# Performance work log

Measured on AMD Instinct MI355X. Metric: run time of the kernel, lower is better.

The kernel has to match this reference:

```python
import jax, jax.numpy as jnp
import numpy as np

ATT_SIZE = 32
HEAD_NUM = 2


def setup_inputs() -> dict:
    key = jax.random.key(0)
    k_in, k_q, k_k, k_v, k_r = jax.random.split(key, 5)
    B, F, D = 16384, 32, 64
    H = ATT_SIZE * HEAD_NUM  # 64
    inputs = jax.random.normal(k_in, (B, F, D), dtype=jnp.float32)
    W_Query = jax.random.truncated_normal(k_q, -2.0, 2.0, (D, H), dtype=jnp.float32) * 0.05
    W_Key = jax.random.truncated_normal(k_k, -2.0, 2.0, (D, H), dtype=jnp.float32) * 0.05
    W_Value = jax.random.truncated_normal(k_v, -2.0, 2.0, (D, H), dtype=jnp.float32) * 0.05
    W_Res = jax.random.truncated_normal(k_r, -2.0, 2.0, (D, H), dtype=jnp.float32) * 0.05
    return {"inputs": inputs, "W_Query": W_Query, "W_Key": W_Key, "W_Value": W_Value, "W_Res": W_Res}


def reference(inputs, W_Query, W_Key, W_Value, W_Res):
    B, F, D = inputs.shape
    h, a = HEAD_NUM, ATT_SIZE
    # project and reshape to [B, h, F, a]
    q = jnp.einsum('bfd,de->bfe', inputs, W_Query).reshape(B, F, h, a).transpose(0, 2, 1, 3)
    k = jnp.einsum('bfd,de->bfe', inputs, W_Key).reshape(B, F, h, a).transpose(0, 2, 1, 3)
    v = jnp.einsum('bfd,de->bfe', inputs, W_Value).reshape(B, F, h, a).transpose(0, 2, 1, 3)
    # NOTE: original code has NO 1/sqrt(d) scaling
    scores = jnp.einsum('bhqa,bhka->bhqk', q, k)
    attn = jax.nn.softmax(scores, axis=-1)
    out = jnp.einsum('bhqk,bhka->bhqa', attn, v)  # [B, h, F, a]
    out = out.transpose(0, 2, 1, 3).reshape(B, F, h * a)
    out = out + jnp.einsum('bfd,de->bfe', inputs, W_Res)
    return jax.nn.relu(out)
```

## Files before the change

kernel.cpp:

```cpp
#include <hip/hip_runtime.h>


constexpr int kF = 32, kD = 64, kH = 64;

using short8   = __attribute__((ext_vector_type(8))) short;
using float4v  = __attribute__((ext_vector_type(4))) float;
using ushort4v = __attribute__((ext_vector_type(4))) unsigned short;

__device__ __forceinline__ unsigned short f2bf(float x) {
    return __builtin_bit_cast(unsigned short, (__bf16)x);
}
__device__ __forceinline__ float bf2f(unsigned short b) {
    return __uint_as_float((unsigned)b << 16);
}
__device__ __forceinline__ int sw64(int row, int blk) {
    return blk ^ ((row ^ (row >> 1)) & 7);
}
__device__ __forceinline__ int sw32(int row, int blk) {
    return blk ^ ((row ^ (row >> 2)) & 3);
}

__global__ void wprep_kernel(const float* __restrict__ Wq, const float* __restrict__ Wk,
                             const float* __restrict__ Wv, const float* __restrict__ Wr,
                             unsigned short* __restrict__ wt) {
    const int m = blockIdx.x;
    const float* __restrict__ W = (m == 0) ? Wq : (m == 1) ? Wk : (m == 2) ? Wv : Wr;
    for (int i = threadIdx.x; i < kD * kH; i += blockDim.x) {
        const int e = i >> 6, d = i & 63;
        wt[m * kD * kH + e * kD + d] = f2bf(W[d * kH + e]);
    }
}

__global__ __launch_bounds__(256, 8)
void interact_mfma(const float* __restrict__ X, const unsigned short* __restrict__ Wt,
                   float* __restrict__ out)
{
    __shared__ __align__(16) unsigned short s_xp[2048];
    __shared__ __align__(16) unsigned short s_q [2048];
    __shared__ __align__(16) unsigned short s_k [2048];
    __shared__ __align__(16) unsigned short s_vt[2048];
    __shared__ __align__(16) unsigned short s_rt[2048];

    const int t    = threadIdx.x;
    const int w    = t >> 6;
    const int lane = t & 63;
    const int quad = lane >> 4;
    const int l    = lane & 15;
    const int b    = blockIdx.x;
    const int h    = w >> 1;
    const int wmt  = w & 1;

    short8 bfrag[4][2];
    {
        const unsigned short* __restrict__ wtm = Wt + w * (kD * kH);
        #pragma unroll
        for (int nt = 0; nt < 4; ++nt)
            #pragma unroll
            for (int ks = 0; ks < 2; ++ks)
                bfrag[nt][ks] =
                    *reinterpret_cast<const short8*>(wtm + (16 * nt + l) * kD + 32 * ks + quad * 8);
    }

    const float* __restrict__ Xb = X + (size_t)b * (kF * kD);
    #pragma unroll
    for (int i = 0; i < 2; ++i) {
        const int idx = i * 256 + t;
        const int f = idx >> 4, c = idx & 15;
        const float4 v = reinterpret_cast<const float4*>(Xb)[idx];
        ushort4v pk = { f2bf(v.x), f2bf(v.y), f2bf(v.z), f2bf(v.w) };
        *reinterpret_cast<ushort4v*>(
            &s_xp[f * 64 + sw64(f, c >> 1) * 8 + (c & 1) * 4]) = pk;
    }
    __syncthreads();

    {
        short8 afrag[2][2];
        #pragma unroll
        for (int mt = 0; mt < 2; ++mt)
            #pragma unroll
            for (int ks = 0; ks < 2; ++ks) {
                const int row = 16 * mt + l;
                afrag[mt][ks] = *reinterpret_cast<const short8*>(
                    &s_xp[row * 64 + sw64(row, 4 * ks + quad) * 8]);
            }

        float4v acc[2][4];
        #pragma unroll
        for (int mt = 0; mt < 2; ++mt)
            #pragma unroll
            for (int nt = 0; nt < 4; ++nt)
                acc[mt][nt] = (float4v){0.f, 0.f, 0.f, 0.f};

        #pragma unroll
        for (int mt = 0; mt < 2; ++mt)
            #pragma unroll
            for (int nt = 0; nt < 4; ++nt) {
                acc[mt][nt] = __builtin_amdgcn_mfma_f32_16x16x32_bf16(
                    afrag[mt][0], bfrag[nt][0], acc[mt][nt], 0, 0, 0);
                acc[mt][nt] = __builtin_amdgcn_mfma_f32_16x16x32_bf16(
                    afrag[mt][1], bfrag[nt][1], acc[mt][nt], 0, 0, 0);
            }

        if (w < 2) {
            unsigned short* __restrict__ dst = (w == 0) ? s_q : s_k;
            #pragma unroll
            for (int mt = 0; mt < 2; ++mt)
                #pragma unroll
                for (int nt = 0; nt < 4; ++nt)
                    #pragma unroll
                    for (int r = 0; r < 4; ++r) {
                        const int row = 16 * mt + quad * 4 + r;
                        dst[row * 64 + sw64(row, 2 * nt + (l >> 3)) * 8 + (l & 7)] =
                            f2bf(acc[mt][nt][r]);
                    }
        } else {
            unsigned short* __restrict__ dstT = (w == 2) ? s_vt : s_rt;
            #pragma unroll
            for (int mt = 0; mt < 2; ++mt)
                #pragma unroll
                for (int nt = 0; nt < 4; ++nt) {
                    const int e = 16 * nt + l;
                    ushort4v pk = { f2bf(acc[mt][nt][0]), f2bf(acc[mt][nt][1]),
                                    f2bf(acc[mt][nt][2]), f2bf(acc[mt][nt][3]) };
                    *reinterpret_cast<ushort4v*>(
                        &dstT[e * 32 + sw32(e, 2 * mt + (quad >> 1)) * 8 + (quad & 1) * 4]) = pk;
                }
        }
    }
    __syncthreads();

    {
        const int qrow = 16 * wmt + l;
        const short8 qa = *reinterpret_cast<const short8*>(
            &s_q[qrow * 64 + sw64(qrow, 4 * h + quad) * 8]);
        const short8 kb0 = *reinterpret_cast<const short8*>(
            &s_k[l * 64 + sw64(l, 4 * h + quad) * 8]);
        const short8 kb1 = *reinterpret_cast<const short8*>(
            &s_k[(16 + l) * 64 + sw64(16 + l, 4 * h + quad) * 8]);

        float4v s0 = (float4v){0.f, 0.f, 0.f, 0.f};
        float4v s1 = (float4v){0.f, 0.f, 0.f, 0.f};
        s0 = __builtin_amdgcn_mfma_f32_16x16x32_bf16(qa, kb0, s0, 0, 0, 0);
        s1 = __builtin_amdgcn_mfma_f32_16x16x32_bf16(qa, kb1, s1, 0, 0, 0);

        #pragma unroll
        for (int r = 0; r < 4; ++r) {
            const int rowG = h * kF + 16 * wmt + quad * 4 + r;
            s_xp[rowG * 32 + sw32(rowG, l >> 3) * 8 + (l & 7)]       = f2bf(__expf(s0[r]));
            s_xp[rowG * 32 + sw32(rowG, 2 + (l >> 3)) * 8 + (l & 7)] = f2bf(__expf(s1[r]));
        }
    }

    {
        const int prow = h * kF + 16 * wmt + l;
        const short8 pa = *reinterpret_cast<const short8*>(
            &s_xp[prow * 32 + sw32(prow, quad) * 8]);
        const short8 vb0 = *reinterpret_cast<const short8*>(
            &s_vt[(32 * h + l) * 32 + sw32(32 * h + l, quad) * 8]);
        const short8 vb1 = *reinterpret_cast<const short8*>(
            &s_vt[(32 * h + 16 + l) * 32 + sw32(32 * h + 16 + l, quad) * 8]);
        const short8 ones = (short8)(short)0x3F80;

        float4v o0 = (float4v){0.f, 0.f, 0.f, 0.f};
        float4v o1 = (float4v){0.f, 0.f, 0.f, 0.f};
        float4v os = (float4v){0.f, 0.f, 0.f, 0.f};
        o0 = __builtin_amdgcn_mfma_f32_16x16x32_bf16(pa, vb0, o0, 0, 0, 0);
        o1 = __builtin_amdgcn_mfma_f32_16x16x32_bf16(pa, vb1, o1, 0, 0, 0);
        os = __builtin_amdgcn_mfma_f32_16x16x32_bf16(pa, ones, os, 0, 0, 0);

        const ushort4v rA = *reinterpret_cast<const ushort4v*>(
            &s_rt[(32 * h + l) * 32 + sw32(32 * h + l, 2 * wmt + (quad >> 1)) * 8 + (quad & 1) * 4]);
        const ushort4v rB = *reinterpret_cast<const ushort4v*>(
            &s_rt[(32 * h + 16 + l) * 32 + sw32(32 * h + 16 + l, 2 * wmt + (quad >> 1)) * 8 + (quad & 1) * 4]);

        float* __restrict__ Ob = out + (size_t)b * (kF * kH);
        #pragma unroll
        for (int r = 0; r < 4; ++r) {
            const int f = 16 * wmt + quad * 4 + r;
            const float inv = __builtin_amdgcn_rcpf(os[r]);
            Ob[f * kH + 32 * h + l]      = fmaxf(o0[r] * inv + bf2f(rA[r]), 0.0f);
            Ob[f * kH + 32 * h + 16 + l] = fmaxf(o1[r] * inv + bf2f(rB[r]), 0.0f);
        }
    }
}

extern "C" void kernel_launch(void* const* d_in, const int* in_sizes, int n_in,
                              void* d_out, int out_size, void* d_ws, size_t ws_size,
                              hipStream_t stream) {
    const float* X  = (const float*)d_in[0];
    const float* Wq = (const float*)d_in[1];
    const float* Wk = (const float*)d_in[2];
    const float* Wv = (const float*)d_in[3];
    const float* Wr = (const float*)d_in[4];
    float* out = (float*)d_out;
    unsigned short* wt = (unsigned short*)d_ws;

    wprep_kernel<<<4, 256, 0, stream>>>(Wq, Wk, Wv, Wr, wt);

    const int B = in_sizes[0] / (kF * kD);
    interact_mfma<<<B, 256, 0, stream>>>(X, wt, out);
}
```

Baseline: 278.3 us.

## Process several batches per block with register prefetch of next input

```diff
diff --git a/kernel.cpp b/kernel.cpp
--- a/kernel.cpp
+++ b/kernel.cpp
@@ -2,6 +2,7 @@
 
 
 constexpr int kF = 32, kD = 64, kH = 64;
+constexpr int NB = 8;
 
 using short8   = __attribute__((ext_vector_type(8))) short;
 using float4v  = __attribute__((ext_vector_type(4))) float;
@@ -46,9 +47,12 @@
     const int lane = t & 63;
     const int quad = lane >> 4;
     const int l    = lane & 15;
-    const int b    = blockIdx.x;
     const int h    = w >> 1;
     const int wmt  = w & 1;
+    const int b0   = blockIdx.x * NB;
+
+    const int f0 = t >> 4,          c0 = t & 15;
+    const int f1 = (256 + t) >> 4,  c1 = t & 15;
 
     short8 bfrag[4][2];
     {
@@ -61,125 +65,145 @@
                     *reinterpret_cast<const short8*>(wtm + (16 * nt + l) * kD + 32 * ks + quad * 8);
     }
 
-    const float* __restrict__ Xb = X + (size_t)b * (kF * kD);
-    #pragma unroll
-    for (int i = 0; i < 2; ++i) {
-        const int idx = i * 256 + t;
-        const int f = idx >> 4, c = idx & 15;
-        const float4 v = reinterpret_cast<const float4*>(Xb)[idx];
-        ushort4v pk = { f2bf(v.x), f2bf(v.y), f2bf(v.z), f2bf(v.w) };
-        *reinterpret_cast<ushort4v*>(
-            &s_xp[f * 64 + sw64(f, c >> 1) * 8 + (c & 1) * 4]) = pk;
-    }
-    __syncthreads();
-
+    float4 xv0, xv1;
     {
-        short8 afrag[2][2];
-        #pragma unroll
-        for (int mt = 0; mt < 2; ++mt)
-            #pragma unroll
-            for (int ks = 0; ks < 2; ++ks) {
-                const int row = 16 * mt + l;
-                afrag[mt][ks] = *reinterpret_cast<const short8*>(
-                    &s_xp[row * 64 + sw64(row, 4 * ks + quad) * 8]);
-            }
-
-        float4v acc[2][4];
-        #pragma unroll
-        for (int mt = 0; mt < 2; ++mt)
-            #pragma unroll
-            for (int nt = 0; nt < 4; ++nt)
-                acc[mt][nt] = (float4v){0.f, 0.f, 0.f, 0.f};
-
-        #pragma unroll
-        for (int mt = 0; mt < 2; ++mt)
-            #pragma unroll
-            for (int nt = 0; nt < 4; ++nt) {
-                acc[mt][nt] = __builtin_amdgcn_mfma_f32_16x16x32_bf16(
-                    afrag[mt][0], bfrag[nt][0], acc[mt][nt], 0, 0, 0);
-                acc[mt][nt] = __builtin_amdgcn_mfma_f32_16x16x32_bf16(
-                    afrag[mt][1], bfrag[nt][1], acc[mt][nt], 0, 0, 0);
-            }
-
-        if (w < 2) {
-            unsigned short* __restrict__ dst = (w == 0) ? s_q : s_k;
+        const float* __restrict__ Xb = X + (size_t)b0 * (kF * kD);
+        xv0 = reinterpret_cast<const float4*>(Xb)[t];
+        xv1 = reinterpret_cast<const float4*>(Xb)[256 + t];
+        ushort4v p0 = { f2bf(xv0.x), f2bf(xv0.y), f2bf(xv0.z), f2bf(xv0.w) };
+        ushort4v p1 = { f2bf(xv1.x), f2bf(xv1.y), f2bf(xv1.z), f2bf(xv1.w) };
+        *reinterpret_cast<ushort4v*>(&s_xp[f0 * 64 + sw64(f0, c0 >> 1) * 8 + (c0 & 1) * 4]) = p0;
+        *reinterpret_cast<ushort4v*>(&s_xp[f1 * 64 + sw64(f1, c1 >> 1) * 8 + (c1 & 1) * 4]) = p1;
+    }
+
+    for (int it = 0; it < NB; ++it) {
+        const int b = b0 + it;
+        __syncthreads();
+
+        {
+            short8 afrag[2][2];
             #pragma unroll
             for (int mt = 0; mt < 2; ++mt)
                 #pragma unroll
+                for (int ks = 0; ks < 2; ++ks) {
+                    const int row = 16 * mt + l;
+                    afrag[mt][ks] = *reinterpret_cast<const short8*>(
+                        &s_xp[row * 64 + sw64(row, 4 * ks + quad) * 8]);
+                }
+
+            if (it + 1 < NB) {
+                const float* __restrict__ Xn = X + (size_t)(b + 1) * (kF * kD);
+                xv0 = reinterpret_cast<const float4*>(Xn)[t];
+                xv1 = reinterpret_cast<const float4*>(Xn)[256 + t];
+            }
+
+            float4v acc[2][4];
+            #pragma unroll
+            for (int mt = 0; mt < 2; ++mt)
+                #pragma unroll
                 for (int nt = 0; nt < 4; ++nt)
+                    acc[mt][nt] = (float4v){0.f, 0.f, 0.f, 0.f};
+
+            #pragma unroll
+            for (int mt = 0; mt < 2; ++mt)
+                #pragma unroll
+                for (int nt = 0; nt < 4; ++nt) {
+                    acc[mt][nt] = __builtin_amdgcn_mfma_f32_16x16x32_bf16(
+                        afrag[mt][0], bfrag[nt][0], acc[mt][nt], 0, 0, 0);
+                    acc[mt][nt] = __builtin_amdgcn_mfma_f32_16x16x32_bf16(
+                        afrag[mt][1], bfrag[nt][1], acc[mt][nt], 0, 0, 0);
+                }
+
+            if (w < 2) {
+                unsigned short* __restrict__ dst = (w == 0) ? s_q : s_k;
+                #pragma unroll
+                for (int mt = 0; mt < 2; ++mt)
                     #pragma unroll
-                    for (int r = 0; r < 4; ++r) {
-                        const int row = 16 * mt + quad * 4 + r;
-                        dst[row * 64 + sw64(row, 2 * nt + (l >> 3)) * 8 + (l & 7)] =
-                            f2bf(acc[mt][nt][r]);
+                    for (int nt = 0; nt < 4; ++nt)
+                        #pragma unroll
+                        for (int r = 0; r < 4; ++r) {
+                            const int row = 16 * mt + quad * 4 + r;
+                            dst[row * 64 + sw64(row, 2 * nt + (l >> 3)) * 8 + (l & 7)] =
+                                f2bf(acc[mt][nt][r]);
+                        }
+            } else {
+                unsigned short* __restrict__ dstT = (w == 2) ? s_vt : s_rt;
+                #pragma unroll
+                for (int mt = 0; mt < 2; ++mt)
+                    #pragma unroll
+                    for (int nt = 0; nt < 4; ++nt) {
+                        const int e = 16 * nt + l;
+                        ushort4v pk = { f2bf(acc[mt][nt][0]), f2bf(acc[mt][nt][1]),
+                                        f2bf(acc[mt][nt][2]), f2bf(acc[mt][nt][3]) };
+                        *reinterpret_cast<ushort4v*>(
+                            &dstT[e * 32 + sw32(e, 2 * mt + (quad >> 1)) * 8 + (quad & 1) * 4]) = pk;
                     }
-        } else {
-            unsigned short* __restrict__ dstT = (w == 2) ? s_vt : s_rt;
-            #pragma unroll
-            for (int mt = 0; mt < 2; ++mt)
-                #pragma unroll
-                for (int nt = 0; nt < 4; ++nt) {
-                    const int e = 16 * nt + l;
-                    ushort4v pk = { f2bf(acc[mt][nt][0]), f2bf(acc[mt][nt][1]),
-                                    f2bf(acc[mt][nt][2]), f2bf(acc[mt][nt][3]) };
-                    *reinterpret_cast<ushort4v*>(
-                        &dstT[e * 32 + sw32(e, 2 * mt + (quad >> 1)) * 8 + (quad & 1) * 4]) = pk;
-                }
-        }
-    }
-    __syncthreads();
-
-    {
-        const int qrow = 16 * wmt + l;
-        const short8 qa = *reinterpret_cast<const short8*>(
-            &s_q[qrow * 64 + sw64(qrow, 4 * h + quad) * 8]);
-        const short8 kb0 = *reinterpret_cast<const short8*>(
-            &s_k[l * 64 + sw64(l, 4 * h + quad) * 8]);
-        const short8 kb1 = *reinterpret_cast<const short8*>(
-            &s_k[(16 + l) * 64 + sw64(16 + l, 4 * h + quad) * 8]);
-
-        float4v s0 = (float4v){0.f, 0.f, 0.f, 0.f};
-        float4v s1 = (float4v){0.f, 0.f, 0.f, 0.f};
-        s0 = __builtin_amdgcn_mfma_f32_16x16x32_bf16(qa, kb0, s0, 0, 0, 0);
-        s1 = __builtin_amdgcn_mfma_f32_16x16x32_bf16(qa, kb1, s1, 0, 0, 0);
-
-        #pragma unroll
-        for (int r = 0; r < 4; ++r) {
-            const int rowG = h * kF + 16 * wmt + quad * 4 + r;
-            s_xp[rowG * 32 + sw32(rowG, l >> 3) * 8 + (l & 7)]       = f2bf(__expf(s0[r]));
-            s_xp[rowG * 32 + sw32(rowG, 2 + (l >> 3)) * 8 + (l & 7)] = f2bf(__expf(s1[r]));
-        }
-    }
-
-    {
-        const int prow = h * kF + 16 * wmt + l;
-        const short8 pa = *reinterpret_cast<const short8*>(
-            &s_xp[prow * 32 + sw32(prow, quad) * 8]);
-        const short8 vb0 = *reinterpret_cast<const short8*>(
-            &s_vt[(32 * h + l) * 32 + sw32(32 * h + l, quad) * 8]);
-        const short8 vb1 = *reinterpret_cast<const short8*>(
-            &s_vt[(32 * h + 16 + l) * 32 + sw32(32 * h + 16 + l, quad) * 8]);
-        const short8 ones = (short8)(short)0x3F80;
-
-        float4v o0 = (float4v){0.f, 0.f, 0.f, 0.f};
-        float4v o1 = (float4v){0.f, 0.f, 0.f, 0.f};
-        float4v os = (float4v){0.f, 0.f, 0.f, 0.f};
-        o0 = __builtin_amdgcn_mfma_f32_16x16x32_bf16(pa, vb0, o0, 0, 0, 0);
-        o1 = __builtin_amdgcn_mfma_f32_16x16x32_bf16(pa, vb1, o1, 0, 0, 0);
-        os = __builtin_amdgcn_mfma_f32_16x16x32_bf16(pa, ones, os, 0, 0, 0);
-
-        const ushort4v rA = *reinterpret_cast<const ushort4v*>(
-            &s_rt[(32 * h + l) * 32 + sw32(32 * h + l, 2 * wmt + (quad >> 1)) * 8 + (quad & 1) * 4]);
-        const ushort4v rB = *reinterpret_cast<const ushort4v*>(
-            &s_rt[(32 * h + 16 + l) * 32 + sw32(32 * h + 16 + l, 2 * wmt + (quad >> 1)) * 8 + (quad & 1) * 4]);
-
-        float* __restrict__ Ob = out + (size_t)b * (kF * kH);
-        #pragma unroll
-        for (int r = 0; r < 4; ++r) {
-            const int f = 16 * wmt + quad * 4 + r;
-            const float inv = __builtin_amdgcn_rcpf(os[r]);
-            Ob[f * kH + 32 * h + l]      = fmaxf(o0[r] * inv + bf2f(rA[r]), 0.0f);
-            Ob[f * kH + 32 * h + 16 + l] = fmaxf(o1[r] * inv + bf2f(rB[r]), 0.0f);
+            }
+        }
+        __syncthreads();
+
+        {
+            const int qrow = 16 * wmt + l;
+            const short8 qa = *reinterpret_cast<const short8*>(
+                &s_q[qrow * 64 + sw64(qrow, 4 * h + quad) * 8]);
+            const short8 kb0 = *reinterpret_cast<const short8*>(
+                &s_k[l * 64 + sw64(l, 4 * h + quad) * 8]);
+            const short8 kb1 = *reinterpret_cast<const short8*>(
+                &s_k[(16 + l) * 64 + sw64(16 + l, 4 * h + quad) * 8]);
+
+            float4v s0 = (float4v){0.f, 0.f, 0.f, 0.f};
+            float4v s1 = (float4v){0.f, 0.f, 0.f, 0.f};
+            s0 = __builtin_amdgcn_mfma_f32_16x16x32_bf16(qa, kb0, s0, 0, 0, 0);
+            s1 = __builtin_amdgcn_mfma_f32_16x16x32_bf16(qa, kb1, s1, 0, 0, 0);
+
+            #pragma unroll
+            for (int r = 0; r < 4; ++r) {
+                const int rowG = h * kF + 16 * wmt + quad * 4 + r;
+                s_xp[rowG * 32 + sw32(rowG, l >> 3) * 8 + (l & 7)]       = f2bf(__expf(s0[r]));
+                s_xp[rowG * 32 + sw32(rowG, 2 + (l >> 3)) * 8 + (l & 7)] = f2bf(__expf(s1[r]));
+            }
+        }
+
+        {
+            const int prow = h * kF + 16 * wmt + l;
+            const short8 pa = *reinterpret_cast<const short8*>(
+                &s_xp[prow * 32 + sw32(prow, quad) * 8]);
+            const short8 vb0 = *reinterpret_cast<const short8*>(
+                &s_vt[(32 * h + l) * 32 + sw32(32 * h + l, quad) * 8]);
+            const short8 vb1 = *reinterpret_cast<const short8*>(
+                &s_vt[(32 * h + 16 + l) * 32 + sw32(32 * h + 16 + l, quad) * 8]);
+            const short8 ones = (short8)(short)0x3F80;
+
+            float4v o0 = (float4v){0.f, 0.f, 0.f, 0.f};
+            float4v o1 = (float4v){0.f, 0.f, 0.f, 0.f};
+            float4v os = (float4v){0.f, 0.f, 0.f, 0.f};
+            o0 = __builtin_amdgcn_mfma_f32_16x16x32_bf16(pa, vb0, o0, 0, 0, 0);
+            o1 = __builtin_amdgcn_mfma_f32_16x16x32_bf16(pa, vb1, o1, 0, 0, 0);
+            os = __builtin_amdgcn_mfma_f32_16x16x32_bf16(pa, ones, os, 0, 0, 0);
+
+            const ushort4v rA = *reinterpret_cast<const ushort4v*>(
+                &s_rt[(32 * h + l) * 32 +
+                      sw32(32 * h + l, 2 * wmt + (quad >> 1)) * 8 + (quad & 1) * 4]);
+            const ushort4v rB = *reinterpret_cast<const ushort4v*>(
+                &s_rt[(32 * h + 16 + l) * 32 +
+                      sw32(32 * h + 16 + l, 2 * wmt + (quad >> 1)) * 8 + (quad & 1) * 4]);
+
+            float* __restrict__ Ob = out + (size_t)b * (kF * kH);
+            #pragma unroll
+            for (int r = 0; r < 4; ++r) {
+                const int f = 16 * wmt + quad * 4 + r;
+                const float inv = __builtin_amdgcn_rcpf(os[r]);
+                Ob[f * kH + 32 * h + l]      = fmaxf(o0[r] * inv + bf2f(rA[r]), 0.0f);
+                Ob[f * kH + 32 * h + 16 + l] = fmaxf(o1[r] * inv + bf2f(rB[r]), 0.0f);
+            }
+        }
+        __syncthreads();
+
+        if (it + 1 < NB) {
+            ushort4v p0 = { f2bf(xv0.x), f2bf(xv0.y), f2bf(xv0.z), f2bf(xv0.w) };
+            ushort4v p1 = { f2bf(xv1.x), f2bf(xv1.y), f2bf(xv1.z), f2bf(xv1.w) };
+            *reinterpret_cast<ushort4v*>(&s_xp[f0 * 64 + sw64(f0, c0 >> 1) * 8 + (c0 & 1) * 4]) = p0;
+            *reinterpret_cast<ushort4v*>(&s_xp[f1 * 64 + sw64(f1, c1 >> 1) * 8 + (c1 & 1) * 4]) = p1;
         }
     }
 }
@@ -198,5 +222,5 @@
     wprep_kernel<<<4, 256, 0, stream>>>(Wq, Wk, Wv, Wr, wt);
 
     const int B = in_sizes[0] / (kF * kD);
-    interact_mfma<<<B, 256, 0, stream>>>(X, wt, out);
-}
+    interact_mfma<<<B / NB, 256, 0, stream>>>(X, wt, out);
+}
```

Result: slower. 454.9 us (+63.5%).
